# Kernel tuning notes

Measured on AMD Instinct MI355X. Metric: run time of the kernel, lower is better.

Reference implementation:

```python
import jax, jax.numpy as jnp
import numpy as np
import math

N, C_IN, H, W = 8, 64, 128, 128
C_OUT, K = 128, 5
MU = 0.9

def _masks():
    _mu = (1.0 - MU) / 3.0
    neighbor = jnp.array([
        [0, _mu, 0, _mu, 0],
        [_mu, _mu, _mu, _mu, _mu],
        [0, _mu, 0, _mu, 0],
        [_mu, _mu, _mu, _mu, _mu],
        [0, _mu, 0, _mu, 0]], dtype=jnp.float32)
    dilator = jnp.array([
        [1.0, 0.0, 1.0, 0.0, 1.0],
        [0.0, 0.0, 0.0, 0.0, 0.0],
        [1.0, 0.0, 1.0, 0.0, 1.0],
        [0.0, 0.0, 0.0, 0.0, 0.0],
        [1.0, 0.0, 1.0, 0.0, 1.0]], dtype=jnp.float32)
    return neighbor, dilator

def setup_inputs() -> dict:
    key = jax.random.key(0)
    k1, k2 = jax.random.split(key)
    input_ = jax.random.normal(k1, (N, C_IN, H, W), dtype=jnp.float32)
    stdv = 1.0 / math.sqrt(C_IN * K * K)
    weight = jax.random.uniform(k2, (C_OUT, C_IN, K, K), dtype=jnp.float32,
                                minval=-stdv, maxval=stdv)
    return {"input_": input_, "weight": weight}

def reference(input_, weight):
    # Faithful math: f_kernel = weight * dilator_mask + neighbor_weight_mask,
    # then a standard 5x5 conv (stride=1, pad=2, dilation=1). The original
    # realizes the conv via F.unfold + matmul (im2col); conv_general_dilated
    # computes identical values. Bias exists as a parameter but is never
    # applied in the original forward, so it is omitted here.
    neighbor, dilator = _masks()
    f_kernel = weight * dilator + neighbor  # broadcast over (O, I)
    out = jax.lax.conv_general_dilated(
        input_, f_kernel,
        window_strides=(1, 1),
        padding=((2, 2), (2, 2)),
        rhs_dilation=(1, 1),
        dimension_numbers=("NCHW", "OIHW", "NCHW"))
    return out  # [N, C_OUT, H, W]
```

## Files before the change

### kernel.cpp

```cpp
#include <hip/hip_runtime.h>

typedef short short8 __attribute__((ext_vector_type(8)));
typedef float f32x4 __attribute__((ext_vector_type(4)));

#define NN 8
#define CI 64
#define CO 128
#define HH 128
#define WW 128
#define PH 132
#define PW 132
#define MU 0.033333333333333333f

#define TPY 8
#define TPX 32
#define HR 12
#define HC 36
#define NPOS (HR * HC)

#define WS_W_BYTES (9 * 128 * 64 * 2)
#define WS_T_OFF   WS_W_BYTES
#define WS_T_BYTES (NN * PH * PW * 4)
#define WS_X_OFF   (WS_T_OFF + WS_T_BYTES)
#define WS_X_BYTES ((size_t)NN * PH * PW * CI * 2)
#define WS_NB_OFF  (WS_X_OFF + WS_X_BYTES)
#define WS_TOTAL   (WS_NB_OFF + WS_T_BYTES)

__device__ __forceinline__ unsigned short f2bf(float f) {
  unsigned u = __float_as_uint(f);
  u += 0x7fffu + ((u >> 16) & 1u);
  return (unsigned short)(u >> 16);
}

__device__ __forceinline__ void g2lds16(const void* g, void* l) {
  __builtin_amdgcn_global_load_lds(
      (const __attribute__((address_space(1))) unsigned int*)g,
      (__attribute__((address_space(3))) unsigned int*)l, 16, 0, 0);
}
__device__ __forceinline__ void g2lds4(const void* g, void* l) {
  __builtin_amdgcn_global_load_lds(
      (const __attribute__((address_space(1))) unsigned int*)g,
      (__attribute__((address_space(3))) unsigned int*)l, 4, 0, 0);
}

__global__ __launch_bounds__(256) void prep_kernel(
    const float* __restrict__ in, const float* __restrict__ w,
    unsigned short* __restrict__ ws_w, float* __restrict__ ws_T,
    short8* __restrict__ ws_x) {
  const int b = blockIdx.x, tid = threadIdx.x;
  if (b < 512) {
    __shared__ short8 lx[256][8];
    const int n = b >> 6, pair = b & 63;
    const int px = tid;
    const int r = pair * 2 + (px >> 7), x = px & 127;
    const float* src = in + ((size_t)(n * CI) * HH + r) * WW + x;
    float tsum = 0.f;
    #pragma unroll
    for (int g = 0; g < 8; ++g) {
      short8 pk;
      #pragma unroll
      for (int j = 0; j < 8; ++j) {
        const float v = src[(size_t)(g * 8 + j) * (HH * WW)];
        tsum += v;
        pk[j] = (short)f2bf(v);
      }
      lx[px][g ^ (px & 7)] = pk;
    }
    ws_T[(n * PH + r + 2) * PW + (x + 2)] = tsum;
    __syncthreads();
    #pragma unroll
    for (int it = 0; it < 8; ++it) {
      const int G = it * 256 + tid;
      const int px2 = G >> 3, g2 = G & 7;
      const int r2 = pair * 2 + (px2 >> 7), x2 = px2 & 127;
      ws_x[((size_t)(n * PH + r2 + 2) * PW + (x2 + 2)) * 8 + g2] =
          lx[px2][g2 ^ (px2 & 7)];
    }
  } else if (b < 520) {
    const int n = b - 512;
    const short8 z = {0, 0, 0, 0, 0, 0, 0, 0};
    for (int e = tid; e < 1040 * 8; e += 256) {
      const int px = e >> 3, g = e & 7;
      int y, x;
      if (px < 528) { const int r4 = px / 132; y = (r4 < 2) ? r4 : r4 + 128; x = px - r4 * 132; }
      else { const int q = px - 528; const int c4 = q >> 7; x = (c4 < 2) ? c4 : c4 + 128; y = 2 + (q & 127); }
      ws_x[((size_t)(n * PH + y) * PW + x) * 8 + g] = z;
    }
    for (int e = tid; e < 1040; e += 256) {
      int y, x;
      if (e < 528) { const int r4 = e / 132; y = (r4 < 2) ? r4 : r4 + 128; x = e - r4 * 132; }
      else { const int q = e - 528; const int c4 = q >> 7; x = (c4 < 2) ? c4 : c4 + 128; y = 2 + (q & 127); }
      ws_T[(n * PH + y) * PW + x] = 0.f;
    }
  } else {
    const int el = (b - 520) * 256 + tid;
    const int lane = el & 63;
    const int idx = el >> 6;
    const int ks = idx & 1, cb = (idx >> 1) & 7, tap = idx >> 4;
    const int lo = lane & 15, hi = lane >> 4;
    const int ky = (tap / 3) * 2, kx = (tap % 3) * 2;
    const float* wp = w + (size_t)((cb * 16 + lo) * 64 + ks * 32 + hi * 8) * 25
                        + ky * 5 + kx;
    short8 pk;
    #pragma unroll
    for (int j = 0; j < 8; ++j) pk[j] = (short)f2bf(wp[j * 25]);
    ((short8*)ws_w)[el] = pk;
  }
}

__global__ __launch_bounds__(256) void nb_kernel(
    const float* __restrict__ ws_T, float* __restrict__ ws_nb) {
  const int p = blockIdx.x * 256 + threadIdx.x;
  const int n = p >> 14, yx = p & 16383;
  const int y = yx >> 7, x = yx & 127;
  const float* Tb = ws_T + (size_t)(n * PH + y) * PW + x;
  float s = 0.f;
  #pragma unroll
  for (int ky = 0; ky < 5; ++ky)
    #pragma unroll
    for (int kx = 0; kx < 5; ++kx)
      if ((ky & 1) | (kx & 1)) s += Tb[ky * PW + kx];
  ws_nb[(size_t)(n * PH + y + 2) * PW + (x + 2)] = s * MU;
}

__global__ __launch_bounds__(256, 1) void conv_kernel(
    const unsigned short* __restrict__ ws_w, const float* __restrict__ ws_nb,
    const unsigned short* __restrict__ ws_x, float* __restrict__ out) {
  __shared__ short8 halo[2][NPOS * 8];
  __shared__ float  nbt[2][256];
  __shared__ short8 wl[36 * 64];
  __shared__ short8 dummy[2 * 64];

  const int tid = threadIdx.x;
  const int wave = tid >> 6, lane = tid & 63;
  const int bid = blockIdx.x;
  const int cob = bid >> 6;
  const int idx0 = bid & 63;
  const int lo = lane & 15, hi = lane >> 4;

  for (int k = wave; k < 36; k += 4) {
    const int tap = k >> 2, r = k & 3;
    const short8* g = (const short8*)ws_w + ((tap * 16 + cob * 4 + r) * 64 + lane);
    g2lds16(g, (char*)wl + k * 1024);
  }

  auto issue_unit = [&](int su, int b) {
    const int t = su & 63, n = su >> 6;
    const int ty0 = (t >> 2) * TPY, tx0 = (t & 3) * TPX;
    for (int k = wave; k < 56; k += 4) {
      const int kk = (k < 54) ? k : (k - 54);
      char* dst = (k < 54) ? ((char*)halo[b] + k * 1024)
                           : ((char*)dummy + (k - 54) * 1024);
      const int pos = kk * 8 + (lane >> 3);
      const int r = pos / HC, c = pos - r * HC;
      const int chunk = (lane & 7) ^ (pos & 7);
      const unsigned short* g =
          ws_x + ((size_t)(n * PH + ty0 + r) * PW + (tx0 + c)) * 64 + chunk * 8;
      g2lds16(g, dst);
    }
    {
      const int rr = 2 * wave + (lane >> 5), cc = lane & 31;
      const float* g = ws_nb + (size_t)(n * PH + ty0 + rr + 2) * PW + (tx0 + cc + 2);
      g2lds4(g, (char*)nbt[b] + wave * 256);
    }
  };

  issue_unit(idx0 * 8, 0);
  asm volatile("s_waitcnt vmcnt(0)" ::: "memory");
  __builtin_amdgcn_s_barrier();
  __builtin_amdgcn_sched_barrier(0);

  int cur = 0;
  for (int u = 0; u < 8; ++u) {
    if (u > 0) {
      asm volatile("s_waitcnt vmcnt(8)" ::: "memory");
      __builtin_amdgcn_s_barrier();
      __builtin_amdgcn_sched_barrier(0);
    }
    if (u < 7) issue_unit(idx0 * 8 + u + 1, cur ^ 1);

    const int su = idx0 * 8 + u;
    const int t = su & 63, n = su >> 6;
    const int ty0 = (t >> 2) * TPY, tx0 = (t & 3) * TPX;

    f32x4 acc[2][4];
    #pragma unroll
    for (int f = 0; f < 4; ++f) {
      const int pb = wave * 64 + f * 16;
      const f32x4 nbv =
          *(const f32x4*)&nbt[cur][(pb >> 5) * 32 + (pb & 31) + hi * 4];
      acc[0][f] = nbv;
      acc[1][f] = nbv;
    }

    #pragma unroll
    for (int tap = 0; tap < 9; ++tap) {
      const int ty = (tap / 3) * 2, tx = (tap % 3) * 2;
      #pragma unroll
      for (int ks = 0; ks < 2; ++ks) {
        short8 wf0 = wl[(tap * 4 + 0 + ks) * 64 + lane];
        short8 wf1 = wl[(tap * 4 + 2 + ks) * 64 + lane];
        #pragma unroll
        for (int f = 0; f < 4; ++f) {
          const int pb = wave * 64 + f * 16;
          const int pos = ((pb >> 5) + ty) * HC + ((pb & 31) + lo + tx);
          const short8 af = halo[cur][pos * 8 + ((ks * 4 + hi) ^ (pos & 7))];
          acc[0][f] = __builtin_amdgcn_mfma_f32_16x16x32_bf16(
              af, wf0, acc[0][f], 0, 0, 0);
          acc[1][f] = __builtin_amdgcn_mfma_f32_16x16x32_bf16(
              af, wf1, acc[1][f], 0, 0, 0);
        }
      }
    }

    #pragma unroll
    for (int cb = 0; cb < 2; ++cb) {
      #pragma unroll
      for (int f = 0; f < 4; ++f) {
        const int pb = wave * 64 + f * 16;
        const int gy = ty0 + (pb >> 5);
        const int gx = tx0 + (pb & 31) + hi * 4;
        const int co = cob * 32 + cb * 16 + lo;
        *(f32x4*)&out[(((size_t)n * CO + co) * HH + gy) * WW + gx] = acc[cb][f];
      }
    }
    cur ^= 1;
  }
}

__global__ __launch_bounds__(256) void prep_kernel_safe(
    const float* __restrict__ in, const float* __restrict__ w,
    unsigned short* __restrict__ ws_w, float* __restrict__ ws_T) {
  const int bid = blockIdx.x, tid = threadIdx.x;
  if (bid < 288) {
    const int el = bid * 256 + tid;
    const int tap = el >> 13;
    const int rem = el & 8191;
    const int co = rem >> 6, ic = rem & 63;
    const int ky = (tap / 3) * 2, kx = (tap % 3) * 2;
    ws_w[el] = f2bf(w[(co * 64 + ic) * 25 + ky * 5 + kx]);
  } else {
    const int p = (bid - 288) * 256 + tid;
    const int n = p >> 14;
    const int yx = p & 16383;
    const float* base = in + (size_t)n * CI * (HH * WW) + yx;
    float s = 0.f;
    #pragma unroll
    for (int ic = 0; ic < CI; ++ic) s += base[ic * (HH * WW)];
    ws_T[p] = s;
  }
}

#define SHR 12
#define SHC 36
#define SNPOS (SHR * SHC)

__global__ __launch_bounds__(256, 2) void conv_kernel_safe(
    const float* __restrict__ in, const unsigned short* __restrict__ ws_w,
    const float* __restrict__ ws_T, float* __restrict__ out) {
  __shared__ short8 in_lds[SNPOS * 8];
  __shared__ float T_lds[SNPOS];

  const int tid = threadIdx.x;
  const int t = blockIdx.x;
  const int n = blockIdx.y;
  const int ty0 = (t >> 2) * 8;
  const int tx0 = (t & 3) * 32;

  for (int e = tid; e < SNPOS * 8; e += 256) {
    const int slot = e / SNPOS;
    const int pos = e - slot * SNPOS;
    const int r = pos / SHC, c = pos - r * SHC;
    const int gy = ty0 + r - 2, gx = tx0 + c - 2;
    const bool ok = (gy >= 0 && gy < HH && gx >= 0 && gx < WW);
    const long off = ((long)(n * CI + slot * 8) * HH + gy) * WW + gx;
    short8 pk;
    #pragma unroll
    for (int j = 0; j < 8; ++j) {
      const float v = ok ? in[off + (long)j * (HH * WW)] : 0.f;
      pk[j] = (short)f2bf(v);
    }
    in_lds[pos * 8 + (slot ^ (pos & 7))] = pk;
  }
  for (int e = tid; e < SNPOS; e += 256) {
    const int r = e / SHC, c = e - r * SHC;
    const int gy = ty0 + r - 2, gx = tx0 + c - 2;
    T_lds[e] = (gy >= 0 && gy < HH && gx >= 0 && gx < WW)
                   ? ws_T[((size_t)n * HH + gy) * WW + gx] : 0.f;
  }
  __syncthreads();

  const int wave = tid >> 6;
  const int lane = tid & 63;
  const int lo = lane & 15;
  const int hi = lane >> 4;

  int py[4], pxc[4];
  #pragma unroll
  for (int f = 0; f < 4; ++f) {
    const int pb = wave * 64 + f * 16;
    py[f] = pb >> 5;
    pxc[f] = (pb & 31) + lo;
  }

  f32x4 acc[8][4];
  #pragma unroll
  for (int cb = 0; cb < 8; ++cb)
    #pragma unroll
    for (int f = 0; f < 4; ++f) acc[cb][f] = (f32x4){0.f, 0.f, 0.f, 0.f};

  const short8* wsv = (const short8*)ws_w;

  #pragma unroll
  for (int tap = 0; tap < 9; ++tap) {
    const int ty = (tap / 3) * 2, tx = (tap % 3) * 2;
    #pragma unroll
    for (int ks = 0; ks < 2; ++ks) {
      short8 bfrag[4];
      #pragma unroll
      for (int f = 0; f < 4; ++f) {
        const int pos = (py[f] + ty) * SHC + (pxc[f] + tx);
        bfrag[f] = in_lds[pos * 8 + ((ks * 4 + hi) ^ (pos & 7))];
      }
      #pragma unroll
      for (int cb = 0; cb < 8; ++cb) {
        const short8 afrag = wsv[(tap * 128 + cb * 16 + lo) * 8 + ks * 4 + hi];
        #pragma unroll
        for (int f = 0; f < 4; ++f)
          acc[cb][f] = __builtin_amdgcn_mfma_f32_16x16x32_bf16(
              afrag, bfrag[f], acc[cb][f], 0, 0, 0);
      }
    }
  }

  float nb[4];
  #pragma unroll
  for (int f = 0; f < 4; ++f) {
    float s = 0.f;
    #pragma unroll
    for (int ky = 0; ky < 5; ++ky)
      #pragma unroll
      for (int kx = 0; kx < 5; ++kx)
        if ((ky & 1) | (kx & 1))
          s += T_lds[(py[f] + ky) * SHC + (pxc[f] + kx)];
    nb[f] = s * MU;
  }

  #pragma unroll
  for (int cb = 0; cb < 8; ++cb) {
    #pragma unroll
    for (int f = 0; f < 4; ++f) {
      const int gy = ty0 + py[f];
      const int gx = tx0 + pxc[f];
      #pragma unroll
      for (int q = 0; q < 4; ++q) {
        const int co = cb * 16 + hi * 4 + q;
        out[(((size_t)n * CO + co) * HH + gy) * WW + gx] = acc[cb][f][q] + nb[f];
      }
    }
  }
}

extern "C" void kernel_launch(void* const* d_in, const int* in_sizes, int n_in,
                              void* d_out, int out_size, void* d_ws, size_t ws_size,
                              hipStream_t stream) {
  const float* in = (const float*)d_in[0];
  const float* w  = (const float*)d_in[1];
  float* out = (float*)d_out;
  unsigned short* ws_w = (unsigned short*)d_ws;

  if (ws_size >= WS_TOTAL) {
    float* ws_T = (float*)((char*)d_ws + WS_T_OFF);
    short8* ws_x = (short8*)((char*)d_ws + WS_X_OFF);
    float* ws_nb = (float*)((char*)d_ws + WS_NB_OFF);
    prep_kernel<<<dim3(556), 256, 0, stream>>>(in, w, ws_w, ws_T, ws_x);
    nb_kernel<<<dim3(512), 256, 0, stream>>>(ws_T, ws_nb);
    conv_kernel<<<dim3(256), 256, 0, stream>>>(
        ws_w, ws_nb, (const unsigned short*)ws_x, out);
  } else {
    float* ws_T = (float*)((char*)d_ws + WS_W_BYTES);
    prep_kernel_safe<<<dim3(288 + 512), 256, 0, stream>>>(in, w, ws_w, ws_T);
    conv_kernel_safe<<<dim3(64, NN), 256, 0, stream>>>(in, ws_w, ws_T, out);
  }
}
```

Measured before the change: 51.96 us.

## Use smaller 4x32 tiles with more blocks and two blocks per CU

The conv kernel's spatial tile shrinks from 8x32 to 4x32 pixels, and the grid grows from 256 to 1024 blocks with launch bounds allowing two blocks per CU. The double-buffered async prefetch pipeline is removed in favour of a simple load, sync, compute, sync loop over four units per block. The aim is to hide memory latency through occupancy and more blocks rather than explicit pipelining. In exchange, each block reloads the full weight set for only four units, and the smaller tile means more halo overhead per output pixel.

Measured after the change: 49.29 us. -5.1%, faster.

```diff
diff --git a/kernel.cpp b/kernel.cpp
--- a/kernel.cpp
+++ b/kernel.cpp
@@ -11,12 +11,6 @@
 #define PH 132
 #define PW 132
 #define MU 0.033333333333333333f
-
-#define TPY 8
-#define TPX 32
-#define HR 12
-#define HC 36
-#define NPOS (HR * HC)
 
 #define WS_W_BYTES (9 * 128 * 64 * 2)
 #define WS_T_OFF   WS_W_BYTES
@@ -123,19 +117,18 @@
   ws_nb[(size_t)(n * PH + y + 2) * PW + (x + 2)] = s * MU;
 }
 
-__global__ __launch_bounds__(256, 1) void conv_kernel(
+__global__ __launch_bounds__(256, 2) void conv_kernel(
     const unsigned short* __restrict__ ws_w, const float* __restrict__ ws_nb,
     const unsigned short* __restrict__ ws_x, float* __restrict__ out) {
-  __shared__ short8 halo[2][NPOS * 8];
-  __shared__ float  nbt[2][256];
+  __shared__ short8 halo[288 * 8];
   __shared__ short8 wl[36 * 64];
-  __shared__ short8 dummy[2 * 64];
+  __shared__ float  nbt[128];
 
   const int tid = threadIdx.x;
   const int wave = tid >> 6, lane = tid & 63;
   const int bid = blockIdx.x;
-  const int cob = bid >> 6;
-  const int idx0 = bid & 63;
+  const int cob = bid >> 8;
+  const int s   = bid & 255;
   const int lo = lane & 15, hi = lane >> 4;
 
   for (int k = wave; k < 36; k += 4) {
@@ -144,51 +137,32 @@
     g2lds16(g, (char*)wl + k * 1024);
   }
 
-  auto issue_unit = [&](int su, int b) {
-    const int t = su & 63, n = su >> 6;
-    const int ty0 = (t >> 2) * TPY, tx0 = (t & 3) * TPX;
-    for (int k = wave; k < 56; k += 4) {
-      const int kk = (k < 54) ? k : (k - 54);
-      char* dst = (k < 54) ? ((char*)halo[b] + k * 1024)
-                           : ((char*)dummy + (k - 54) * 1024);
-      const int pos = kk * 8 + (lane >> 3);
-      const int r = pos / HC, c = pos - r * HC;
+  for (int j = 0; j < 4; ++j) {
+    const int su = s * 4 + j;
+    const int n = su >> 7, rem = su & 127;
+    const int ty0 = (rem >> 2) * 4;
+    const int tx0 = (rem & 3) * 32;
+
+    for (int k = wave; k < 36; k += 4) {
+      const int pos = k * 8 + (lane >> 3);
+      const int r = pos / 36, c = pos - r * 36;
       const int chunk = (lane & 7) ^ (pos & 7);
       const unsigned short* g =
           ws_x + ((size_t)(n * PH + ty0 + r) * PW + (tx0 + c)) * 64 + chunk * 8;
-      g2lds16(g, dst);
-    }
-    {
-      const int rr = 2 * wave + (lane >> 5), cc = lane & 31;
-      const float* g = ws_nb + (size_t)(n * PH + ty0 + rr + 2) * PW + (tx0 + cc + 2);
-      g2lds4(g, (char*)nbt[b] + wave * 256);
-    }
-  };
-
-  issue_unit(idx0 * 8, 0);
-  asm volatile("s_waitcnt vmcnt(0)" ::: "memory");
-  __builtin_amdgcn_s_barrier();
-  __builtin_amdgcn_sched_barrier(0);
-
-  int cur = 0;
-  for (int u = 0; u < 8; ++u) {
-    if (u > 0) {
-      asm volatile("s_waitcnt vmcnt(8)" ::: "memory");
-      __builtin_amdgcn_s_barrier();
-      __builtin_amdgcn_sched_barrier(0);
-    }
-    if (u < 7) issue_unit(idx0 * 8 + u + 1, cur ^ 1);
-
-    const int su = idx0 * 8 + u;
-    const int t = su & 63, n = su >> 6;
-    const int ty0 = (t >> 2) * TPY, tx0 = (t & 3) * TPX;
-
-    f32x4 acc[2][4];
-    #pragma unroll
-    for (int f = 0; f < 4; ++f) {
-      const int pb = wave * 64 + f * 16;
-      const f32x4 nbv =
-          *(const f32x4*)&nbt[cur][(pb >> 5) * 32 + (pb & 31) + hi * 4];
+      g2lds16(g, (char*)halo + k * 1024);
+    }
+    if (wave < 2) {
+      const float* g = ws_nb
+          + (size_t)(n * PH + ty0 + 2 * wave + (lane >> 5) + 2) * PW
+          + (tx0 + (lane & 31) + 2);
+      g2lds4(g, (char*)nbt + wave * 256);
+    }
+    __syncthreads();
+
+    f32x4 acc[2][2];
+    #pragma unroll
+    for (int f = 0; f < 2; ++f) {
+      const f32x4 nbv = *(const f32x4*)&nbt[wave * 32 + f * 16 + hi * 4];
       acc[0][f] = nbv;
       acc[1][f] = nbv;
     }
@@ -198,13 +172,12 @@
       const int ty = (tap / 3) * 2, tx = (tap % 3) * 2;
       #pragma unroll
       for (int ks = 0; ks < 2; ++ks) {
-        short8 wf0 = wl[(tap * 4 + 0 + ks) * 64 + lane];
-        short8 wf1 = wl[(tap * 4 + 2 + ks) * 64 + lane];
+        const short8 wf0 = wl[(tap * 4 + 0 + ks) * 64 + lane];
+        const short8 wf1 = wl[(tap * 4 + 2 + ks) * 64 + lane];
         #pragma unroll
-        for (int f = 0; f < 4; ++f) {
-          const int pb = wave * 64 + f * 16;
-          const int pos = ((pb >> 5) + ty) * HC + ((pb & 31) + lo + tx);
-          const short8 af = halo[cur][pos * 8 + ((ks * 4 + hi) ^ (pos & 7))];
+        for (int f = 0; f < 2; ++f) {
+          const int pos = (wave + ty) * 36 + (f * 16 + lo + tx);
+          const short8 af = halo[pos * 8 + ((ks * 4 + hi) ^ (pos & 7))];
           acc[0][f] = __builtin_amdgcn_mfma_f32_16x16x32_bf16(
               af, wf0, acc[0][f], 0, 0, 0);
           acc[1][f] = __builtin_amdgcn_mfma_f32_16x16x32_bf16(
@@ -216,15 +189,14 @@
     #pragma unroll
     for (int cb = 0; cb < 2; ++cb) {
       #pragma unroll
-      for (int f = 0; f < 4; ++f) {
-        const int pb = wave * 64 + f * 16;
-        const int gy = ty0 + (pb >> 5);
-        const int gx = tx0 + (pb & 31) + hi * 4;
+      for (int f = 0; f < 2; ++f) {
+        const int gy = ty0 + wave;
+        const int gx = tx0 + f * 16 + hi * 4;
         const int co = cob * 32 + cb * 16 + lo;
         *(f32x4*)&out[(((size_t)n * CO + co) * HH + gy) * WW + gx] = acc[cb][f];
       }
     }
-    cur ^= 1;
+    __syncthreads();
   }
 }
 
@@ -375,7 +347,7 @@
     float* ws_nb = (float*)((char*)d_ws + WS_NB_OFF);
     prep_kernel<<<dim3(556), 256, 0, stream>>>(in, w, ws_w, ws_T, ws_x);
     nb_kernel<<<dim3(512), 256, 0, stream>>>(ws_T, ws_nb);
-    conv_kernel<<<dim3(256), 256, 0, stream>>>(
+    conv_kernel<<<dim3(1024), 256, 0, stream>>>(
         ws_w, ws_nb, (const unsigned short*)ws_x, out);
   } else {
     float* ws_T = (float*)((char*)d_ws + WS_W_BYTES);
```
